# Performance work log

Hardware: AMD Instinct MI355X
Metric: run time of the kernel (lower is better)

Reference implementation:

```python
import jax, jax.numpy as jnp
import numpy as np

N, E, NC = 50000, 800000, 5
H, C = 4, 16      # branch GATConvs: heads=4, out=16 -> 64
H2, C2 = 4, 32    # conv2/conv3: heads=4, out=32 -> 128
HID = 128


def _gat(x, src, dst, W, a_s, a_d, b, mask=None, edge_attr=None, We=None, a_e=None):
    """PyG-style GATConv with add_self_loops=True (fill_value='mean' for edge_attr)."""
    n = x.shape[0]
    h, c = a_s.shape
    hx = (x @ W).reshape(n, h, c)                      # [N,H,C]
    as_n = (hx * a_s).sum(-1)                          # [N,H]
    ad_n = (hx * a_d).sum(-1)                          # [N,H]
    alpha = as_n[src] + ad_n[dst]                      # [E,H]
    loop = as_n + ad_n                                 # self-loop scores [N,H]
    if edge_attr is not None:
        ee = (edge_attr @ We).reshape(-1, h, c)        # [E,H,C]
        alpha = alpha + (ee * a_e).sum(-1)
        w = mask.astype(x.dtype) if mask is not None else jnp.ones((edge_attr.shape[0],), x.dtype)
        # fill_value='mean': self-loop attr = mean of (masked) incoming edge_attr
        loop_attr = jax.ops.segment_sum(edge_attr * w[:, None], dst, n) / \
                    jnp.maximum(jax.ops.segment_sum(w, dst, n), 1.0)[:, None]
        loop = loop + ((loop_attr @ We).reshape(n, h, c) * a_e).sum(-1)
    alpha = jax.nn.leaky_relu(alpha, 0.2)
    loop = jax.nn.leaky_relu(loop, 0.2)
    if mask is not None:
        alpha = jnp.where(mask[:, None], alpha, -jnp.inf)
    # segment softmax over destination neighborhoods (self-loop always present)
    m = jnp.maximum(jax.ops.segment_max(alpha, dst, n), loop)      # [N,H], finite
    ex = jnp.exp(alpha - m[dst])                                   # [E,H]
    if mask is not None:
        ex = jnp.where(mask[:, None], ex, 0.0)
    exl = jnp.exp(loop - m)                                        # [N,H]
    denom = jax.ops.segment_sum(ex, dst, n) + exl
    out = jax.ops.segment_sum(ex[:, :, None] * hx[src], dst, n) + exl[:, :, None] * hx
    return (out / denom[:, :, None]).reshape(n, h * c) + b


def setup_inputs() -> dict:
    key = jax.random.key(0)
    ks = iter(jax.random.split(key, 64))
    def nrm(shape, s=0.1):
        return jax.random.normal(next(ks), shape, jnp.float32) * s
    d = {}
    d["x"] = nrm((N, 1), 1.0)
    d["edge_index"] = jax.random.randint(next(ks), (2, E), 0, N, jnp.int32)
    d["edge_attr"] = nrm((E, 3), 1.0)
    d["mask_t"] = jax.random.randint(next(ks), (E,), 0, 2, jnp.int32).astype(bool)
    d["mask_g"] = jax.random.randint(next(ks), (E,), 0, 2, jnp.int32).astype(bool)
    d["mask_p"] = jax.random.randint(next(ks), (E,), 0, 2, jnp.int32).astype(bool)
    for p in ("t", "g", "p"):
        d[f"W{p}"] = nrm((1, H * C))
        d[f"a{p}s"] = nrm((H, C)); d[f"a{p}d"] = nrm((H, C)); d[f"a{p}e"] = nrm((H, C))
        d[f"W{p}e"] = nrm((3, H * C))
        d[f"b{p}"] = jnp.zeros((H * C,), jnp.float32)
    d["Wf"] = nrm((3 * H * C, HID)); d["bf"] = jnp.zeros((HID,), jnp.float32)
    d["W2"] = nrm((HID, H2 * C2)); d["a2s"] = nrm((H2, C2)); d["a2d"] = nrm((H2, C2)); d["b2"] = jnp.zeros((H2 * C2,), jnp.float32)
    d["W3"] = nrm((HID, H2 * C2)); d["a3s"] = nrm((H2, C2)); d["a3d"] = nrm((H2, C2)); d["b3"] = jnp.zeros((H2 * C2,), jnp.float32)
    d["Wc1"] = nrm((HID, HID // 2)); d["bc1"] = jnp.zeros((HID // 2,), jnp.float32)
    d["Wc2"] = nrm((HID // 2, NC)); d["bc2"] = jnp.zeros((NC,), jnp.float32)
    return d


def reference(x, edge_index, edge_attr, mask_t, mask_g, mask_p,
              Wt, ats, atd, ate, Wte, bt,
              Wg, ags, agd, age, Wge, bg,
              Wp, aps, apd, ape, Wpe, bp,
              Wf, bf, W2, a2s, a2d, b2, W3, a3s, a3d, b3,
              Wc1, bc1, Wc2, bc2):
    src, dst = edge_index[0], edge_index[1]
    ht = _gat(x, src, dst, Wt, ats, atd, bt, mask_t, edge_attr, Wte, ate)
    hg = _gat(x, src, dst, Wg, ags, agd, bg, mask_g, edge_attr, Wge, age)
    hp = _gat(x, src, dst, Wp, aps, apd, bp, mask_p, edge_attr, Wpe, ape)
    h = jax.nn.relu(jnp.concatenate([ht, hg, hp], -1) @ Wf + bf)
    h = jax.nn.relu(_gat(h, src, dst, W2, a2s, a2d, b2))
    h = jax.nn.relu(_gat(h, src, dst, W3, a3s, a3d, b3))
    logits = jax.nn.relu(h @ Wc1 + bc1) @ Wc2 + bc2
    return jax.nn.log_softmax(logits, -1)
```

## Files before the change

### kernel.cpp

```cpp
#include <hip/hip_runtime.h>
#include <hip/hip_bf16.h>

#define LEAKY(v) ((v) > 0.f ? (v) : 0.2f * (v))

typedef __attribute__((ext_vector_type(8))) short s8;
typedef __attribute__((ext_vector_type(4))) float f4;
typedef __attribute__((ext_vector_type(4))) unsigned short us4;

__device__ __forceinline__ unsigned short f_to_bf16(float f) {
    union { float f; unsigned int i; } v; v.f = f;
    unsigned int x = v.i;
    return (unsigned short)((x + 0x7fffu + ((x >> 16) & 1u)) >> 16);
}

__device__ __forceinline__ float2 bf2_to_f2(unsigned int u) {
    union { unsigned int i; float f; } a, b;
    a.i = (u & 0xffffu) << 16;
    b.i = u & 0xffff0000u;
    float2 r; r.x = a.f; r.y = b.f;
    return r;
}

struct ConstBuf {
    float ws[3][4];
    float wd[3][4];
    float M[3][3][4];
    float G[12][128];
    float bias2[128];
};
#define CB_FLOATS 1724

struct BranchW { const float *W, *as_, *ad_, *ae, *We, *b; };
struct PreArgs { BranchW br[3]; const float *Wf, *bf; ConstBuf* cb; };

__global__ void k_precompute(PreArgs A) {
    int t = threadIdx.x;
    if (t < 24) {
        int b = t / 8, r = t % 8, h = r & 3; bool isd = r >= 4;
        const float* a = isd ? A.br[b].ad_ : A.br[b].as_;
        float s = 0.f;
        for (int c = 0; c < 16; ++c) s += A.br[b].W[h * 16 + c] * a[h * 16 + c];
        if (isd) A.cb->wd[b][h] = s; else A.cb->ws[b][h] = s;
    }
    if (t >= 32 && t < 68) {
        int id = t - 32, b = id / 12, k = (id % 12) / 4, h = id & 3;
        float s = 0.f;
        for (int c = 0; c < 16; ++c) s += A.br[b].We[k * 64 + h * 16 + c] * A.br[b].ae[h * 16 + c];
        A.cb->M[b][k][h] = s;
    }
    if (t >= 128) {
        int j = t - 128;
        float s = A.bf[j];
        for (int b = 0; b < 3; ++b)
            for (int i = 0; i < 64; ++i)
                s += A.br[b].b[i] * A.Wf[(b * 64 + i) * 128 + j];
        A.cb->bias2[j] = s;
    }
    for (int id = t; id < 1536; id += 256) {
        int r = id >> 7, j = id & 127, b = r >> 2, h = r & 3;
        float s = 0.f;
        for (int c = 0; c < 16; ++c)
            s += A.br[b].W[h * 16 + c] * A.Wf[(b * 64 + h * 16 + c) * 128 + j];
        A.cb->G[r][j] = s;
    }
}

__global__ void k_prepw(const float* __restrict__ W, unsigned short* __restrict__ out) {
    for (int i = threadIdx.x; i < 16384; i += 256) {
        int j = i & 7, lane = (i >> 3) & 63, kk = (i >> 9) & 3, ct = i >> 11;
        int k = kk * 32 + (lane >> 4) * 8 + j;
        int n = ct * 16 + (lane & 15);
        out[i] = f_to_bf16(W[k * 128 + n]);
    }
}

__global__ void k_count(const int* __restrict__ ei, int E, int* __restrict__ deg) {
    int e = blockIdx.x * blockDim.x + threadIdx.x;
    if (e < E) atomicAdd(&deg[ei[E + e]], 1);
}

#define SCAN_EPB 2048

__global__ void k_scan1(const int* __restrict__ deg, int* __restrict__ off,
                        int* __restrict__ partials, int total) {
    __shared__ int sd[256];
    int t = threadIdx.x;
    int base = blockIdx.x * SCAN_EPB + t * 8;
    int v[8];
    int s = 0;
    #pragma unroll
    for (int i = 0; i < 8; ++i) {
        int idx = base + i;
        v[i] = (idx < total - 1) ? deg[idx] : 0;
        s += v[i];
    }
    sd[t] = s;
    __syncthreads();
    #pragma unroll
    for (int ofs = 1; ofs < 256; ofs <<= 1) {
        int u = (t >= ofs) ? sd[t - ofs] : 0;
        __syncthreads();
        sd[t] += u;
        __syncthreads();
    }
    if (t == 255) partials[blockIdx.x] = sd[255];
    int run = sd[t] - s;
    #pragma unroll
    for (int i = 0; i < 8; ++i) {
        int idx = base + i;
        if (idx < total) off[idx] = run;
        run += v[i];
    }
}

__global__ void k_scan2(int* __restrict__ partials, int nb) {
    __shared__ int sd[256];
    int t = threadIdx.x;
    int v = (t < nb) ? partials[t] : 0;
    sd[t] = v;
    __syncthreads();
    #pragma unroll
    for (int ofs = 1; ofs < 256; ofs <<= 1) {
        int u = (t >= ofs) ? sd[t - ofs] : 0;
        __syncthreads();
        sd[t] += u;
        __syncthreads();
    }
    if (t < nb) partials[t] = sd[t] - v;
}

__global__ void k_scan3(int* __restrict__ off, const int* __restrict__ partials,
                        int* __restrict__ cursor, int total) {
    int idx = blockIdx.x * blockDim.x + threadIdx.x;
    if (idx < total) {
        int v = off[idx] + partials[idx / SCAN_EPB];
        off[idx] = v;
        if (idx < total - 1) cursor[idx] = v;
    }
}

__global__ void k_scatter(const int* __restrict__ ei, const float* __restrict__ attr,
                          const int* __restrict__ mt, const int* __restrict__ mg,
                          const int* __restrict__ mp, int E, int* __restrict__ cursor,
                          float4* __restrict__ rec) {
    int e = blockIdx.x * blockDim.x + threadIdx.x;
    if (e < E) {
        int d = ei[E + e];
        int p = atomicAdd(&cursor[d], 1);
        float4 r;
        r.x = attr[e * 3 + 0];
        r.y = attr[e * 3 + 1];
        r.z = attr[e * 3 + 2];
        unsigned int bits = (mt[e] != 0 ? 1u : 0u) | (mg[e] != 0 ? 2u : 0u) | (mp[e] != 0 ? 4u : 0u);
        unsigned int packed = (unsigned int)ei[e] | (bits << 16);
        r.w = __int_as_float((int)packed);
        rec[p] = r;
    }
}

__global__ void k_branch(const float* __restrict__ x, const int* __restrict__ off,
                         const float4* __restrict__ rec, int* __restrict__ csr_src,
                         const ConstBuf* __restrict__ cb, float* __restrict__ h1, int N) {
    __shared__ float sc[CB_FLOATS];
    for (int i = threadIdx.x; i < CB_FLOATS; i += 256) sc[i] = ((const float*)cb)[i];
    __syncthreads();
    int g = threadIdx.x >> 4, l = threadIdx.x & 15;
    int n = blockIdx.x * 16 + g;
    if (n >= N) return;

    float num[12], den[12], asum[9], cnt[3];
    #pragma unroll
    for (int i = 0; i < 12; ++i) { num[i] = 0.f; den[i] = 0.f; }
    #pragma unroll
    for (int i = 0; i < 9; ++i) asum[i] = 0.f;
    cnt[0] = cnt[1] = cnt[2] = 0.f;

    float xn = x[n];
    int beg = off[n], end = off[n + 1];
    for (int p = beg + l; p < end; p += 16) {
        float4 r = rec[p];
        unsigned int packed = (unsigned int)__float_as_int(r.w);
        int src = (int)(packed & 0xffffu);
        unsigned int bits = packed >> 16;
        csr_src[p] = src;
        float xs = x[src];
        float a0 = r.x, a1 = r.y, a2 = r.z;
        #pragma unroll
        for (int b = 0; b < 3; ++b) {
            if ((bits >> b) & 1u) {
                cnt[b] += 1.f;
                asum[b * 3 + 0] += a0; asum[b * 3 + 1] += a1; asum[b * 3 + 2] += a2;
                #pragma unroll
                for (int h = 0; h < 4; ++h) {
                    float al = xs * sc[b * 4 + h] + xn * sc[12 + b * 4 + h]
                             + a0 * sc[24 + b * 12 + 0 + h]
                             + a1 * sc[24 + b * 12 + 4 + h]
                             + a2 * sc[24 + b * 12 + 8 + h];
                    al = LEAKY(al);
                    float ex = __expf(al);
                    den[b * 4 + h] += ex;
                    num[b * 4 + h] += ex * xs;
                }
            }
        }
    }
    #pragma unroll
    for (int m = 1; m < 16; m <<= 1) {
        #pragma unroll
        for (int i = 0; i < 12; ++i) {
            num[i] += __shfl_xor(num[i], m, 64);
            den[i] += __shfl_xor(den[i], m, 64);
        }
        #pragma unroll
        for (int i = 0; i < 9; ++i) asum[i] += __shfl_xor(asum[i], m, 64);
        #pragma unroll
        for (int i = 0; i < 3; ++i) cnt[i] += __shfl_xor(cnt[i], m, 64);
    }
    float S[12];
    #pragma unroll
    for (int b = 0; b < 3; ++b) {
        float inv = 1.f / fmaxf(cnt[b], 1.f);
        float l0 = asum[b * 3 + 0] * inv, l1 = asum[b * 3 + 1] * inv, l2 = asum[b * 3 + 2] * inv;
        #pragma unroll
        for (int h = 0; h < 4; ++h) {
            float lp = xn * (sc[b * 4 + h] + sc[12 + b * 4 + h])
                     + l0 * sc[24 + b * 12 + 0 + h]
                     + l1 * sc[24 + b * 12 + 4 + h]
                     + l2 * sc[24 + b * 12 + 8 + h];
            lp = LEAKY(lp);
            float exl = __expf(lp);
            float sden = den[b * 4 + h] + exl;
            S[b * 4 + h] = (num[b * 4 + h] + exl * xn) / sden;
        }
    }
    int jb = l * 8;
    float o[8];
    #pragma unroll
    for (int q = 0; q < 8; ++q) {
        int j = jb + q;
        float a = sc[60 + 1536 + j];
        #pragma unroll
        for (int k = 0; k < 12; ++k) a += S[k] * sc[60 + k * 128 + j];
        o[q] = fmaxf(a, 0.f);
    }
    float4* dst = (float4*)(h1 + (size_t)n * 128 + jb);
    dst[0] = make_float4(o[0], o[1], o[2], o[3]);
    dst[1] = make_float4(o[4], o[5], o[6], o[7]);
}

__global__ void k_mm128b(const float* __restrict__ A, const unsigned short* __restrict__ wf,
                         unsigned short* __restrict__ hxb, int N) {
    __shared__ unsigned short sA[64 * 136];
    __shared__ unsigned short sW[16384];
    int tid = threadIdx.x;
    int base = blockIdx.x * 64;
    const float4* wf4 = (const float4*)wf;
    float4* sW4 = (float4*)sW;
    #pragma unroll
    for (int i = 0; i < 8; ++i) sW4[tid + i * 256] = wf4[tid + i * 256];
    #pragma unroll
    for (int i = 0; i < 8; ++i) {
        int f = tid + i * 256;
        int row = f >> 5, c4 = f & 31;
        int n = base + row;
        float4 v = (n < N) ? ((const float4*)A)[(size_t)n * 32 + c4]
                           : make_float4(0.f, 0.f, 0.f, 0.f);
        us4 b;
        b.x = f_to_bf16(v.x); b.y = f_to_bf16(v.y);
        b.z = f_to_bf16(v.z); b.w = f_to_bf16(v.w);
        *(us4*)(&sA[row * 136 + c4 * 4]) = b;
    }
    __syncthreads();
    int wv = tid >> 6, lane = tid & 63;
    int q = lane >> 4, l15 = lane & 15;
    int rowbase = wv * 16;
    s8 af[4];
    #pragma unroll
    for (int kk = 0; kk < 4; ++kk)
        af[kk] = *(const s8*)(&sA[(rowbase + l15) * 136 + kk * 32 + q * 8]);
    #pragma unroll
    for (int ct = 0; ct < 8; ++ct) {
        f4 acc = {0.f, 0.f, 0.f, 0.f};
        #pragma unroll
        for (int kk = 0; kk < 4; ++kk) {
            s8 bfr = *(const s8*)(&sW[((ct * 4 + kk) * 64 + lane) * 8]);
            acc = __builtin_amdgcn_mfma_f32_16x16x32_bf16(af[kk], bfr, acc, 0, 0, 0);
        }
        #pragma unroll
        for (int r = 0; r < 4; ++r) {
            int n = base + rowbase + q * 4 + r;
            if (n < N) hxb[(size_t)n * 128 + ct * 16 + l15] = f_to_bf16(acc[r]);
        }
    }
}

__global__ void k_scoresb(const unsigned short* __restrict__ hxb, const float* __restrict__ a_s,
                          const float* __restrict__ a_d, float* __restrict__ as_,
                          float* __restrict__ ad_, int N) {
    __shared__ float sas[128], sad[128];
    if (threadIdx.x < 128) { sas[threadIdx.x] = a_s[threadIdx.x]; sad[threadIdx.x] = a_d[threadIdx.x]; }
    __syncthreads();
    int tid = blockIdx.x * blockDim.x + threadIdx.x;
    int n = tid >> 2, h = tid & 3;
    if (n >= N) return;
    const uint4* r4 = (const uint4*)(hxb + (size_t)n * 128 + h * 32);
    float ss = 0.f, sd2 = 0.f;
    #pragma unroll
    for (int c = 0; c < 4; ++c) {
        uint4 blob = r4[c];
        unsigned int us[4] = { blob.x, blob.y, blob.z, blob.w };
        #pragma unroll
        for (int q = 0; q < 4; ++q) {
            float2 v = bf2_to_f2(us[q]);
            int col = h * 32 + c * 8 + q * 2;
            ss  += v.x * sas[col] + v.y * sas[col + 1];
            sd2 += v.x * sad[col] + v.y * sad[col + 1];
        }
    }
    as_[(size_t)n * 4 + h] = ss;
    ad_[(size_t)n * 4 + h] = sd2;
}

__global__ void k_gatagg(const unsigned short* __restrict__ hxb, const float* __restrict__ as_,
                         const float* __restrict__ ad_, const float* __restrict__ b,
                         const int* __restrict__ off, const int* __restrict__ csr_src,
                         float* __restrict__ out, int N) {
    int wave = threadIdx.x >> 6, lane = threadIdx.x & 63;
    int n = blockIdx.x * 4 + wave;
    if (n >= N) return;
    int h = lane >> 4;
    int lofs = lane * 2;
    float adn = ad_[(size_t)n * 4 + h];
    int beg = off[n], end = off[n + 1];
    float acc0 = 0.f, acc1 = 0.f, accd = 0.f;
    for (int p = beg; p < end; p += 8) {
        int s[8]; float e[8]; unsigned int u[8]; bool valid[8];
        #pragma unroll
        for (int i = 0; i < 8; ++i) {
            valid[i] = (p + i < end);
            int q = valid[i] ? (p + i) : beg;
            s[i] = csr_src[q];
        }
        #pragma unroll
        for (int i = 0; i < 8; ++i) e[i] = as_[(size_t)s[i] * 4 + h];
        #pragma unroll
        for (int i = 0; i < 8; ++i) u[i] = *(const unsigned int*)(hxb + (size_t)s[i] * 128 + lofs);
        #pragma unroll
        for (int i = 0; i < 8; ++i) {
            float ex = valid[i] ? __expf(LEAKY(e[i] + adn)) : 0.f;
            float2 v = bf2_to_f2(u[i]);
            acc0 += ex * v.x; acc1 += ex * v.y; accd += ex;
        }
    }
    float aln = LEAKY(as_[(size_t)n * 4 + h] + adn);
    float exl = __expf(aln);
    unsigned int un = *(const unsigned int*)(hxb + (size_t)n * 128 + lofs);
    float2 vn = bf2_to_f2(un);
    float inv = 1.f / (accd + exl);
    float o0 = (acc0 + exl * vn.x) * inv + b[lofs + 0];
    float o1 = (acc1 + exl * vn.y) * inv + b[lofs + 1];
    float2 r; r.x = fmaxf(o0, 0.f); r.y = fmaxf(o1, 0.f);
    *(float2*)(out + (size_t)n * 128 + lofs) = r;
}

#define CLS_NPB 32
__global__ void k_cls(const float* __restrict__ h3, const float* __restrict__ Wc1,
                      const float* __restrict__ bc1, const float* __restrict__ Wc2,
                      const float* __restrict__ bc2, float* __restrict__ out, int N) {
    __shared__ float hs[CLS_NPB * 128];
    int tid = threadIdx.x;
    int nb = blockIdx.x * CLS_NPB;
    for (int i = tid; i < CLS_NPB * 128; i += 256) {
        int n = nb + (i >> 7);
        hs[i] = (n < N) ? h3[(size_t)n * 128 + (i & 127)] : 0.f;
    }
    __syncthreads();
    int g = tid >> 6, j = tid & 63;
    const float4* hb4 = (const float4*)(hs + g * 8 * 128);
    float bj = bc1[j];
    float acc[8];
    #pragma unroll
    for (int i = 0; i < 8; ++i) acc[i] = bj;
    for (int k = 0; k < 128; k += 4) {
        float w0 = Wc1[(k + 0) * 64 + j];
        float w1 = Wc1[(k + 1) * 64 + j];
        float w2 = Wc1[(k + 2) * 64 + j];
        float w3 = Wc1[(k + 3) * 64 + j];
        #pragma unroll
        for (int i = 0; i < 8; ++i) {
            float4 h4 = hb4[(i * 128 + k) >> 2];
            acc[i] += h4.x * w0 + h4.y * w1 + h4.z * w2 + h4.w * w3;
        }
    }
    float w2v[5];
    #pragma unroll
    for (int c = 0; c < 5; ++c) w2v[c] = Wc2[j * 5 + c];
    #pragma unroll
    for (int i = 0; i < 8; ++i) {
        float t = fmaxf(acc[i], 0.f);
        float p[5];
        #pragma unroll
        for (int c = 0; c < 5; ++c) p[c] = t * w2v[c];
        #pragma unroll
        for (int m = 1; m < 64; m <<= 1) {
            #pragma unroll
            for (int c = 0; c < 5; ++c) p[c] += __shfl_xor(p[c], m, 64);
        }
        if (j == 0) {
            int n = nb + g * 8 + i;
            if (n < N) {
                float l[5], mx = -1e30f;
                #pragma unroll
                for (int c = 0; c < 5; ++c) { l[c] = p[c] + bc2[c]; mx = fmaxf(mx, l[c]); }
                float s = 0.f;
                #pragma unroll
                for (int c = 0; c < 5; ++c) s += __expf(l[c] - mx);
                float lse = mx + __logf(s);
                #pragma unroll
                for (int c = 0; c < 5; ++c) out[(size_t)n * 5 + c] = l[c] - lse;
            }
        }
    }
}

extern "C" void kernel_launch(void* const* d_in, const int* in_sizes, int n_in,
                              void* d_out, int out_size, void* d_ws, size_t ws_size,
                              hipStream_t stream) {
    const float* x    = (const float*)d_in[0];
    const int*   ei   = (const int*)d_in[1];
    const float* attr = (const float*)d_in[2];
    const int*   mt   = (const int*)d_in[3];
    const int*   mg   = (const int*)d_in[4];
    const int*   mp   = (const int*)d_in[5];
    const float* Wf   = (const float*)d_in[24];
    const float* bf   = (const float*)d_in[25];
    const float* W2   = (const float*)d_in[26];
    const float* a2s  = (const float*)d_in[27];
    const float* a2d  = (const float*)d_in[28];
    const float* b2   = (const float*)d_in[29];
    const float* W3   = (const float*)d_in[30];
    const float* a3s  = (const float*)d_in[31];
    const float* a3d  = (const float*)d_in[32];
    const float* b3   = (const float*)d_in[33];
    const float* Wc1  = (const float*)d_in[34];
    const float* bc1  = (const float*)d_in[35];
    const float* Wc2  = (const float*)d_in[36];
    const float* bc2  = (const float*)d_in[37];

    int N = in_sizes[0];
    int E = in_sizes[1] / 2;

    char* w = (char*)d_ws;
    auto alloc = [&](size_t bytes) {
        char* p = w;
        w += (bytes + 255) & ~(size_t)255;
        return p;
    };
    int* off      = (int*)alloc((size_t)(N + 1) * 4);
    int* cursor   = (int*)alloc((size_t)N * 4);
    int* deg      = (int*)alloc((size_t)N * 4);
    int* partials = (int*)alloc(1024 * 4);
    int* csr_src  = (int*)alloc((size_t)E * 4);
    ConstBuf* cb  = (ConstBuf*)alloc(sizeof(ConstBuf));
    float* as_    = (float*)alloc((size_t)N * 4 * 4);
    float* ad_    = (float*)alloc((size_t)N * 4 * 4);
    float* bufA   = (float*)alloc((size_t)N * 128 * 4);
    float4* rec   = (float4*)alloc((size_t)E * 16);
    unsigned short* hxb = (unsigned short*)alloc((size_t)N * 256);
    unsigned short* wf2 = (unsigned short*)alloc(16384 * 2);
    unsigned short* wf3 = (unsigned short*)alloc(16384 * 2);

    PreArgs pa;
    for (int b = 0; b < 3; ++b) {
        pa.br[b].W   = (const float*)d_in[6 + b * 6 + 0];
        pa.br[b].as_ = (const float*)d_in[6 + b * 6 + 1];
        pa.br[b].ad_ = (const float*)d_in[6 + b * 6 + 2];
        pa.br[b].ae  = (const float*)d_in[6 + b * 6 + 3];
        pa.br[b].We  = (const float*)d_in[6 + b * 6 + 4];
        pa.br[b].b   = (const float*)d_in[6 + b * 6 + 5];
    }
    pa.Wf = Wf; pa.bf = bf; pa.cb = cb;

    int total = N + 1;
    int nScanBlocks = (total + SCAN_EPB - 1) / SCAN_EPB;

    hipMemsetAsync(deg, 0, (size_t)N * 4, stream);
    hipLaunchKernelGGL(k_precompute, dim3(1), dim3(256), 0, stream, pa);
    hipLaunchKernelGGL(k_prepw, dim3(1), dim3(256), 0, stream, W2, wf2);
    hipLaunchKernelGGL(k_prepw, dim3(1), dim3(256), 0, stream, W3, wf3);
    int gE = (E + 255) / 256;
    hipLaunchKernelGGL(k_count, dim3(gE), dim3(256), 0, stream, ei, E, deg);
    hipLaunchKernelGGL(k_scan1, dim3(nScanBlocks), dim3(256), 0, stream, deg, off, partials, total);
    hipLaunchKernelGGL(k_scan2, dim3(1), dim3(256), 0, stream, partials, nScanBlocks);
    hipLaunchKernelGGL(k_scan3, dim3((total + 255) / 256), dim3(256), 0, stream,
                       off, partials, cursor, total);
    hipLaunchKernelGGL(k_scatter, dim3(gE), dim3(256), 0, stream,
                       ei, attr, mt, mg, mp, E, cursor, rec);
    hipLaunchKernelGGL(k_branch, dim3((N + 15) / 16), dim3(256), 0, stream,
                       x, off, rec, csr_src, cb, bufA, N);
    hipLaunchKernelGGL(k_mm128b, dim3((N + 63) / 64), dim3(256), 0, stream,
                       bufA, wf2, hxb, N);
    hipLaunchKernelGGL(k_scoresb, dim3(((size_t)N * 4 + 255) / 256), dim3(256), 0, stream,
                       hxb, a2s, a2d, as_, ad_, N);
    hipLaunchKernelGGL(k_gatagg, dim3((N + 3) / 4), dim3(256), 0, stream,
                       hxb, as_, ad_, b2, off, csr_src, bufA, N);
    hipLaunchKernelGGL(k_mm128b, dim3((N + 63) / 64), dim3(256), 0, stream,
                       bufA, wf3, hxb, N);
    hipLaunchKernelGGL(k_scoresb, dim3(((size_t)N * 4 + 255) / 256), dim3(256), 0, stream,
                       hxb, a3s, a3d, as_, ad_, N);
    hipLaunchKernelGGL(k_gatagg, dim3((N + 3) / 4), dim3(256), 0, stream,
                       hxb, as_, ad_, b3, off, csr_src, bufA, N);
    hipLaunchKernelGGL(k_cls, dim3((N + CLS_NPB - 1) / CLS_NPB), dim3(256), 0, stream,
                       bufA, Wc1, bc1, Wc2, bc2, (float*)d_out, N);
}
```

Baseline: 461.1 us.

## Merge setup kernels, vectorize edge count/scatter, deepen gather unroll

Folds the three single-block setup kernels into one three-block launch, so the weight conversions run in parallel with the constant precompute and two launches are dropped. The degree count and CSR scatter now handle four edges per thread with int4/float4 loads, cutting per-edge load instructions. The GAT aggregation loop now prefetches 16 neighbors per iteration instead of 8 to expose more memory-level parallelism, at the cost of more registers and possible occupancy loss. The vector path assumes 16-byte aligned pointers and E divisible by 4, with a scalar fallback otherwise.

```diff
diff --git a/kernel.cpp b/kernel.cpp
--- a/kernel.cpp
+++ b/kernel.cpp
@@ -33,50 +33,62 @@
 struct BranchW { const float *W, *as_, *ad_, *ae, *We, *b; };
 struct PreArgs { BranchW br[3]; const float *Wf, *bf; ConstBuf* cb; };
 
-__global__ void k_precompute(PreArgs A) {
+__global__ void k_pre_all(PreArgs A, const float* __restrict__ W2, unsigned short* __restrict__ wf2,
+                          const float* __restrict__ W3, unsigned short* __restrict__ wf3) {
     int t = threadIdx.x;
-    if (t < 24) {
-        int b = t / 8, r = t % 8, h = r & 3; bool isd = r >= 4;
-        const float* a = isd ? A.br[b].ad_ : A.br[b].as_;
-        float s = 0.f;
-        for (int c = 0; c < 16; ++c) s += A.br[b].W[h * 16 + c] * a[h * 16 + c];
-        if (isd) A.cb->wd[b][h] = s; else A.cb->ws[b][h] = s;
-    }
-    if (t >= 32 && t < 68) {
-        int id = t - 32, b = id / 12, k = (id % 12) / 4, h = id & 3;
-        float s = 0.f;
-        for (int c = 0; c < 16; ++c) s += A.br[b].We[k * 64 + h * 16 + c] * A.br[b].ae[h * 16 + c];
-        A.cb->M[b][k][h] = s;
-    }
-    if (t >= 128) {
-        int j = t - 128;
-        float s = A.bf[j];
-        for (int b = 0; b < 3; ++b)
-            for (int i = 0; i < 64; ++i)
-                s += A.br[b].b[i] * A.Wf[(b * 64 + i) * 128 + j];
-        A.cb->bias2[j] = s;
-    }
-    for (int id = t; id < 1536; id += 256) {
-        int r = id >> 7, j = id & 127, b = r >> 2, h = r & 3;
-        float s = 0.f;
-        for (int c = 0; c < 16; ++c)
-            s += A.br[b].W[h * 16 + c] * A.Wf[(b * 64 + h * 16 + c) * 128 + j];
-        A.cb->G[r][j] = s;
-    }
-}
-
-__global__ void k_prepw(const float* __restrict__ W, unsigned short* __restrict__ out) {
-    for (int i = threadIdx.x; i < 16384; i += 256) {
-        int j = i & 7, lane = (i >> 3) & 63, kk = (i >> 9) & 3, ct = i >> 11;
-        int k = kk * 32 + (lane >> 4) * 8 + j;
-        int n = ct * 16 + (lane & 15);
-        out[i] = f_to_bf16(W[k * 128 + n]);
+    if (blockIdx.x == 0) {
+        if (t < 24) {
+            int b = t / 8, r = t % 8, h = r & 3; bool isd = r >= 4;
+            const float* a = isd ? A.br[b].ad_ : A.br[b].as_;
+            float s = 0.f;
+            for (int c = 0; c < 16; ++c) s += A.br[b].W[h * 16 + c] * a[h * 16 + c];
+            if (isd) A.cb->wd[b][h] = s; else A.cb->ws[b][h] = s;
+        }
+        if (t >= 32 && t < 68) {
+            int id = t - 32, b = id / 12, k = (id % 12) / 4, h = id & 3;
+            float s = 0.f;
+            for (int c = 0; c < 16; ++c) s += A.br[b].We[k * 64 + h * 16 + c] * A.br[b].ae[h * 16 + c];
+            A.cb->M[b][k][h] = s;
+        }
+        if (t >= 128) {
+            int j = t - 128;
+            float s = A.bf[j];
+            for (int b = 0; b < 3; ++b)
+                for (int i = 0; i < 64; ++i)
+                    s += A.br[b].b[i] * A.Wf[(b * 64 + i) * 128 + j];
+            A.cb->bias2[j] = s;
+        }
+        for (int id = t; id < 1536; id += 256) {
+            int r = id >> 7, j = id & 127, b = r >> 2, h = r & 3;
+            float s = 0.f;
+            for (int c = 0; c < 16; ++c)
+                s += A.br[b].W[h * 16 + c] * A.Wf[(b * 64 + h * 16 + c) * 128 + j];
+            A.cb->G[r][j] = s;
+        }
+    } else {
+        const float* W = (blockIdx.x == 1) ? W2 : W3;
+        unsigned short* out = (blockIdx.x == 1) ? wf2 : wf3;
+        for (int i = t; i < 16384; i += 256) {
+            int j = i & 7, lane = (i >> 3) & 63, kk = (i >> 9) & 3, ct = i >> 11;
+            int k = kk * 32 + (lane >> 4) * 8 + j;
+            int n = ct * 16 + (lane & 15);
+            out[i] = f_to_bf16(W[k * 128 + n]);
+        }
     }
 }
 
 __global__ void k_count(const int* __restrict__ ei, int E, int* __restrict__ deg) {
-    int e = blockIdx.x * blockDim.x + threadIdx.x;
-    if (e < E) atomicAdd(&deg[ei[E + e]], 1);
+    int base = (blockIdx.x * blockDim.x + threadIdx.x) * 4;
+    if (base >= E) return;
+    if (base + 3 < E && (E & 3) == 0) {
+        int4 d = *(const int4*)(ei + E + base);
+        atomicAdd(&deg[d.x], 1);
+        atomicAdd(&deg[d.y], 1);
+        atomicAdd(&deg[d.z], 1);
+        atomicAdd(&deg[d.w], 1);
+    } else {
+        for (int e = base; e < E && e < base + 4; ++e) atomicAdd(&deg[ei[E + e]], 1);
+    }
 }
 
 #define SCAN_EPB 2048
@@ -143,18 +155,41 @@
                           const int* __restrict__ mt, const int* __restrict__ mg,
                           const int* __restrict__ mp, int E, int* __restrict__ cursor,
                           float4* __restrict__ rec) {
-    int e = blockIdx.x * blockDim.x + threadIdx.x;
-    if (e < E) {
-        int d = ei[E + e];
-        int p = atomicAdd(&cursor[d], 1);
-        float4 r;
-        r.x = attr[e * 3 + 0];
-        r.y = attr[e * 3 + 1];
-        r.z = attr[e * 3 + 2];
-        unsigned int bits = (mt[e] != 0 ? 1u : 0u) | (mg[e] != 0 ? 2u : 0u) | (mp[e] != 0 ? 4u : 0u);
-        unsigned int packed = (unsigned int)ei[e] | (bits << 16);
-        r.w = __int_as_float((int)packed);
-        rec[p] = r;
+    int base = (blockIdx.x * blockDim.x + threadIdx.x) * 4;
+    if (base >= E) return;
+    if (base + 3 < E && (E & 3) == 0) {
+        int4 d4 = *(const int4*)(ei + E + base);
+        int4 s4 = *(const int4*)(ei + base);
+        int4 t4 = *(const int4*)(mt + base);
+        int4 g4 = *(const int4*)(mg + base);
+        int4 p4 = *(const int4*)(mp + base);
+        const float4* a4 = (const float4*)(attr + (size_t)base * 3);
+        float4 a0 = a4[0], a1 = a4[1], a2 = a4[2];
+        int p0 = atomicAdd(&cursor[d4.x], 1);
+        int p1 = atomicAdd(&cursor[d4.y], 1);
+        int p2 = atomicAdd(&cursor[d4.z], 1);
+        int p3 = atomicAdd(&cursor[d4.w], 1);
+        unsigned int b0 = (t4.x ? 1u : 0u) | (g4.x ? 2u : 0u) | (p4.x ? 4u : 0u);
+        unsigned int b1 = (t4.y ? 1u : 0u) | (g4.y ? 2u : 0u) | (p4.y ? 4u : 0u);
+        unsigned int b2 = (t4.z ? 1u : 0u) | (g4.z ? 2u : 0u) | (p4.z ? 4u : 0u);
+        unsigned int b3 = (t4.w ? 1u : 0u) | (g4.w ? 2u : 0u) | (p4.w ? 4u : 0u);
+        float4 r0 = make_float4(a0.x, a0.y, a0.z, __int_as_float((int)((unsigned)s4.x | (b0 << 16))));
+        float4 r1 = make_float4(a0.w, a1.x, a1.y, __int_as_float((int)((unsigned)s4.y | (b1 << 16))));
+        float4 r2 = make_float4(a1.z, a1.w, a2.x, __int_as_float((int)((unsigned)s4.z | (b2 << 16))));
+        float4 r3 = make_float4(a2.y, a2.z, a2.w, __int_as_float((int)((unsigned)s4.w | (b3 << 16))));
+        rec[p0] = r0; rec[p1] = r1; rec[p2] = r2; rec[p3] = r3;
+    } else {
+        for (int e = base; e < E && e < base + 4; ++e) {
+            int d = ei[E + e];
+            int p = atomicAdd(&cursor[d], 1);
+            float4 r;
+            r.x = attr[e * 3 + 0];
+            r.y = attr[e * 3 + 1];
+            r.z = attr[e * 3 + 2];
+            unsigned int bits = (mt[e] != 0 ? 1u : 0u) | (mg[e] != 0 ? 2u : 0u) | (mp[e] != 0 ? 4u : 0u);
+            r.w = __int_as_float((int)((unsigned)ei[e] | (bits << 16)));
+            rec[p] = r;
+        }
     }
 }
 
@@ -333,20 +368,20 @@
     float adn = ad_[(size_t)n * 4 + h];
     int beg = off[n], end = off[n + 1];
     float acc0 = 0.f, acc1 = 0.f, accd = 0.f;
-    for (int p = beg; p < end; p += 8) {
-        int s[8]; float e[8]; unsigned int u[8]; bool valid[8];
-        #pragma unroll
-        for (int i = 0; i < 8; ++i) {
+    for (int p = beg; p < end; p += 16) {
+        int s[16]; float e[16]; unsigned int u[16]; bool valid[16];
+        #pragma unroll
+        for (int i = 0; i < 16; ++i) {
             valid[i] = (p + i < end);
             int q = valid[i] ? (p + i) : beg;
             s[i] = csr_src[q];
         }
         #pragma unroll
-        for (int i = 0; i < 8; ++i) e[i] = as_[(size_t)s[i] * 4 + h];
-        #pragma unroll
-        for (int i = 0; i < 8; ++i) u[i] = *(const unsigned int*)(hxb + (size_t)s[i] * 128 + lofs);
-        #pragma unroll
-        for (int i = 0; i < 8; ++i) {
+        for (int i = 0; i < 16; ++i) e[i] = as_[(size_t)s[i] * 4 + h];
+        #pragma unroll
+        for (int i = 0; i < 16; ++i) u[i] = *(const unsigned int*)(hxb + (size_t)s[i] * 128 + lofs);
+        #pragma unroll
+        for (int i = 0; i < 16; ++i) {
             float ex = valid[i] ? __expf(LEAKY(e[i] + adn)) : 0.f;
             float2 v = bf2_to_f2(u[i]);
             acc0 += ex * v.x; acc1 += ex * v.y; accd += ex;
@@ -485,16 +520,14 @@
     int nScanBlocks = (total + SCAN_EPB - 1) / SCAN_EPB;
 
     hipMemsetAsync(deg, 0, (size_t)N * 4, stream);
-    hipLaunchKernelGGL(k_precompute, dim3(1), dim3(256), 0, stream, pa);
-    hipLaunchKernelGGL(k_prepw, dim3(1), dim3(256), 0, stream, W2, wf2);
-    hipLaunchKernelGGL(k_prepw, dim3(1), dim3(256), 0, stream, W3, wf3);
-    int gE = (E + 255) / 256;
-    hipLaunchKernelGGL(k_count, dim3(gE), dim3(256), 0, stream, ei, E, deg);
+    hipLaunchKernelGGL(k_pre_all, dim3(3), dim3(256), 0, stream, pa, W2, wf2, W3, wf3);
+    int gE4 = (E + 1023) / 1024;
+    hipLaunchKernelGGL(k_count, dim3(gE4), dim3(256), 0, stream, ei, E, deg);
     hipLaunchKernelGGL(k_scan1, dim3(nScanBlocks), dim3(256), 0, stream, deg, off, partials, total);
     hipLaunchKernelGGL(k_scan2, dim3(1), dim3(256), 0, stream, partials, nScanBlocks);
     hipLaunchKernelGGL(k_scan3, dim3((total + 255) / 256), dim3(256), 0, stream,
                        off, partials, cursor, total);
-    hipLaunchKernelGGL(k_scatter, dim3(gE), dim3(256), 0, stream,
+    hipLaunchKernelGGL(k_scatter, dim3(gE4), dim3(256), 0, stream,
                        ei, attr, mt, mg, mp, E, cursor, rec);
     hipLaunchKernelGGL(k_branch, dim3((N + 15) / 16), dim3(256), 0, stream,
                        x, off, rec, csr_src, cb, bufA, N);
```

Measured after the change: 451.7 us. 1.02x faster.

## Merge weight-prep kernels, partition scatter by destination range, deepen gather unroll

Applied to the files above, without the earlier changes.

Three separate changes. The three single-block setup kernels become one three-block launch. The CSR scatter now launches 8x the blocks, and each block handles only destinations within one eighth of the node range, so atomics and record writes land in a narrower region, likely for L2/XCD locality. The GAT aggregation loop now gathers 16 neighbours per iteration instead of 8, exposing more memory-level parallelism at the cost of more registers and more wasted lanes on low-degree nodes.

```diff
diff --git a/kernel.cpp b/kernel.cpp
--- a/kernel.cpp
+++ b/kernel.cpp
@@ -33,44 +33,47 @@
 struct BranchW { const float *W, *as_, *ad_, *ae, *We, *b; };
 struct PreArgs { BranchW br[3]; const float *Wf, *bf; ConstBuf* cb; };
 
-__global__ void k_precompute(PreArgs A) {
+__global__ void k_pre_all(PreArgs A, const float* __restrict__ W2, unsigned short* __restrict__ wf2,
+                          const float* __restrict__ W3, unsigned short* __restrict__ wf3) {
     int t = threadIdx.x;
-    if (t < 24) {
-        int b = t / 8, r = t % 8, h = r & 3; bool isd = r >= 4;
-        const float* a = isd ? A.br[b].ad_ : A.br[b].as_;
-        float s = 0.f;
-        for (int c = 0; c < 16; ++c) s += A.br[b].W[h * 16 + c] * a[h * 16 + c];
-        if (isd) A.cb->wd[b][h] = s; else A.cb->ws[b][h] = s;
-    }
-    if (t >= 32 && t < 68) {
-        int id = t - 32, b = id / 12, k = (id % 12) / 4, h = id & 3;
-        float s = 0.f;
-        for (int c = 0; c < 16; ++c) s += A.br[b].We[k * 64 + h * 16 + c] * A.br[b].ae[h * 16 + c];
-        A.cb->M[b][k][h] = s;
-    }
-    if (t >= 128) {
-        int j = t - 128;
-        float s = A.bf[j];
-        for (int b = 0; b < 3; ++b)
-            for (int i = 0; i < 64; ++i)
-                s += A.br[b].b[i] * A.Wf[(b * 64 + i) * 128 + j];
-        A.cb->bias2[j] = s;
-    }
-    for (int id = t; id < 1536; id += 256) {
-        int r = id >> 7, j = id & 127, b = r >> 2, h = r & 3;
-        float s = 0.f;
-        for (int c = 0; c < 16; ++c)
-            s += A.br[b].W[h * 16 + c] * A.Wf[(b * 64 + h * 16 + c) * 128 + j];
-        A.cb->G[r][j] = s;
-    }
-}
-
-__global__ void k_prepw(const float* __restrict__ W, unsigned short* __restrict__ out) {
-    for (int i = threadIdx.x; i < 16384; i += 256) {
-        int j = i & 7, lane = (i >> 3) & 63, kk = (i >> 9) & 3, ct = i >> 11;
-        int k = kk * 32 + (lane >> 4) * 8 + j;
-        int n = ct * 16 + (lane & 15);
-        out[i] = f_to_bf16(W[k * 128 + n]);
+    if (blockIdx.x == 0) {
+        if (t < 24) {
+            int b = t / 8, r = t % 8, h = r & 3; bool isd = r >= 4;
+            const float* a = isd ? A.br[b].ad_ : A.br[b].as_;
+            float s = 0.f;
+            for (int c = 0; c < 16; ++c) s += A.br[b].W[h * 16 + c] * a[h * 16 + c];
+            if (isd) A.cb->wd[b][h] = s; else A.cb->ws[b][h] = s;
+        }
+        if (t >= 32 && t < 68) {
+            int id = t - 32, b = id / 12, k = (id % 12) / 4, h = id & 3;
+            float s = 0.f;
+            for (int c = 0; c < 16; ++c) s += A.br[b].We[k * 64 + h * 16 + c] * A.br[b].ae[h * 16 + c];
+            A.cb->M[b][k][h] = s;
+        }
+        if (t >= 128) {
+            int j = t - 128;
+            float s = A.bf[j];
+            for (int b = 0; b < 3; ++b)
+                for (int i = 0; i < 64; ++i)
+                    s += A.br[b].b[i] * A.Wf[(b * 64 + i) * 128 + j];
+            A.cb->bias2[j] = s;
+        }
+        for (int id = t; id < 1536; id += 256) {
+            int r = id >> 7, j = id & 127, b = r >> 2, h = r & 3;
+            float s = 0.f;
+            for (int c = 0; c < 16; ++c)
+                s += A.br[b].W[h * 16 + c] * A.Wf[(b * 64 + h * 16 + c) * 128 + j];
+            A.cb->G[r][j] = s;
+        }
+    } else {
+        const float* W = (blockIdx.x == 1) ? W2 : W3;
+        unsigned short* out = (blockIdx.x == 1) ? wf2 : wf3;
+        for (int i = t; i < 16384; i += 256) {
+            int j = i & 7, lane = (i >> 3) & 63, kk = (i >> 9) & 3, ct = i >> 11;
+            int k = kk * 32 + (lane >> 4) * 8 + j;
+            int n = ct * 16 + (lane & 15);
+            out[i] = f_to_bf16(W[k * 128 + n]);
+        }
     }
 }
 
@@ -141,21 +144,22 @@
 
 __global__ void k_scatter(const int* __restrict__ ei, const float* __restrict__ attr,
                           const int* __restrict__ mt, const int* __restrict__ mg,
-                          const int* __restrict__ mp, int E, int* __restrict__ cursor,
-                          float4* __restrict__ rec) {
-    int e = blockIdx.x * blockDim.x + threadIdx.x;
-    if (e < E) {
-        int d = ei[E + e];
-        int p = atomicAdd(&cursor[d], 1);
-        float4 r;
-        r.x = attr[e * 3 + 0];
-        r.y = attr[e * 3 + 1];
-        r.z = attr[e * 3 + 2];
-        unsigned int bits = (mt[e] != 0 ? 1u : 0u) | (mg[e] != 0 ? 2u : 0u) | (mp[e] != 0 ? 4u : 0u);
-        unsigned int packed = (unsigned int)ei[e] | (bits << 16);
-        r.w = __int_as_float((int)packed);
-        rec[p] = r;
-    }
+                          const int* __restrict__ mp, int E, int chunk,
+                          int* __restrict__ cursor, float4* __restrict__ rec) {
+    int r = blockIdx.x & 7;
+    int slice = blockIdx.x >> 3;
+    int e = slice * 256 + threadIdx.x;
+    if (e >= E) return;
+    int d = ei[E + e];
+    if ((unsigned)(d - r * chunk) >= (unsigned)chunk) return;
+    int p = atomicAdd(&cursor[d], 1);
+    float4 rr;
+    rr.x = attr[e * 3 + 0];
+    rr.y = attr[e * 3 + 1];
+    rr.z = attr[e * 3 + 2];
+    unsigned int bits = (mt[e] != 0 ? 1u : 0u) | (mg[e] != 0 ? 2u : 0u) | (mp[e] != 0 ? 4u : 0u);
+    rr.w = __int_as_float((int)((unsigned)ei[e] | (bits << 16)));
+    rec[p] = rr;
 }
 
 __global__ void k_branch(const float* __restrict__ x, const int* __restrict__ off,
@@ -333,20 +337,20 @@
     float adn = ad_[(size_t)n * 4 + h];
     int beg = off[n], end = off[n + 1];
     float acc0 = 0.f, acc1 = 0.f, accd = 0.f;
-    for (int p = beg; p < end; p += 8) {
-        int s[8]; float e[8]; unsigned int u[8]; bool valid[8];
-        #pragma unroll
-        for (int i = 0; i < 8; ++i) {
+    for (int p = beg; p < end; p += 16) {
+        int s[16]; float e[16]; unsigned int u[16]; bool valid[16];
+        #pragma unroll
+        for (int i = 0; i < 16; ++i) {
             valid[i] = (p + i < end);
             int q = valid[i] ? (p + i) : beg;
             s[i] = csr_src[q];
         }
         #pragma unroll
-        for (int i = 0; i < 8; ++i) e[i] = as_[(size_t)s[i] * 4 + h];
-        #pragma unroll
-        for (int i = 0; i < 8; ++i) u[i] = *(const unsigned int*)(hxb + (size_t)s[i] * 128 + lofs);
-        #pragma unroll
-        for (int i = 0; i < 8; ++i) {
+        for (int i = 0; i < 16; ++i) e[i] = as_[(size_t)s[i] * 4 + h];
+        #pragma unroll
+        for (int i = 0; i < 16; ++i) u[i] = *(const unsigned int*)(hxb + (size_t)s[i] * 128 + lofs);
+        #pragma unroll
+        for (int i = 0; i < 16; ++i) {
             float ex = valid[i] ? __expf(LEAKY(e[i] + adn)) : 0.f;
             float2 v = bf2_to_f2(u[i]);
             acc0 += ex * v.x; acc1 += ex * v.y; accd += ex;
@@ -485,17 +489,16 @@
     int nScanBlocks = (total + SCAN_EPB - 1) / SCAN_EPB;
 
     hipMemsetAsync(deg, 0, (size_t)N * 4, stream);
-    hipLaunchKernelGGL(k_precompute, dim3(1), dim3(256), 0, stream, pa);
-    hipLaunchKernelGGL(k_prepw, dim3(1), dim3(256), 0, stream, W2, wf2);
-    hipLaunchKernelGGL(k_prepw, dim3(1), dim3(256), 0, stream, W3, wf3);
+    hipLaunchKernelGGL(k_pre_all, dim3(3), dim3(256), 0, stream, pa, W2, wf2, W3, wf3);
     int gE = (E + 255) / 256;
     hipLaunchKernelGGL(k_count, dim3(gE), dim3(256), 0, stream, ei, E, deg);
     hipLaunchKernelGGL(k_scan1, dim3(nScanBlocks), dim3(256), 0, stream, deg, off, partials, total);
     hipLaunchKernelGGL(k_scan2, dim3(1), dim3(256), 0, stream, partials, nScanBlocks);
     hipLaunchKernelGGL(k_scan3, dim3((total + 255) / 256), dim3(256), 0, stream,
                        off, partials, cursor, total);
-    hipLaunchKernelGGL(k_scatter, dim3(gE), dim3(256), 0, stream,
-                       ei, attr, mt, mg, mp, E, cursor, rec);
+    int chunk = (N + 7) / 8;
+    hipLaunchKernelGGL(k_scatter, dim3(gE * 8), dim3(256), 0, stream,
+                       ei, attr, mt, mg, mp, E, chunk, cursor, rec);
     hipLaunchKernelGGL(k_branch, dim3((N + 15) / 16), dim3(256), 0, stream,
                        x, off, rec, csr_src, cb, bufA, N);
     hipLaunchKernelGGL(k_mm128b, dim3((N + 63) / 64), dim3(256), 0, stream,
```

Result: no change. 454.6 us (-1.4%).
